# Kernel tuning notes

Hardware: AMD Instinct MI355X
Metric: run time of the kernel (lower is better)

The kernel has to match this reference:

```python
import jax, jax.numpy as jnp
import numpy as np

PSEUDO_CONF_THRES = 0.2


def setup_inputs() -> dict:
    key = jax.random.key(0)
    k1, k2, k3, k4 = jax.random.split(key, 4)
    B, S, M = 4096, 10000, 1000  # batch, num_sub_classes, num_main_classes
    x = jax.random.normal(k1, (B, S), dtype=jnp.float32)
    x_main = jax.random.normal(k2, (B, M), dtype=jnp.float32)
    target = jax.random.randint(k3, (B,), 0, S, dtype=jnp.int64)
    sub2main = jax.random.randint(k4, (S,), 0, M, dtype=jnp.int64)
    return {"x": x, "x_main": x_main, "target": target, "sub2main": sub2main}


def _corrected_target(x, x_main, target, sub2main, thres):
    # Vectorized form of _main2sub_corrected_label (original uses detached scores).
    B, S = x.shape
    score_sub = jax.nn.softmax(x, axis=1)            # [B, S]
    score_main = jax.nn.softmax(x_main, axis=1)      # [B, M]
    pseudo = jnp.argmax(score_sub, axis=1)           # [B]
    rows = jnp.arange(B)
    prob_target = score_main[rows, sub2main[target]]   # [B]
    prob_pseudo = score_main[rows, sub2main[pseudo]]   # [B]
    correct = (target != pseudo) & (prob_pseudo >= thres)
    lam_sum = prob_target + prob_pseudo
    lam_t = jnp.where(correct, prob_target / lam_sum, 1.0)
    lam_c = jnp.where(correct, prob_pseudo / lam_sum, 0.0)
    one_hot = jnp.zeros((B, S), dtype=x.dtype)
    one_hot = one_hot.at[rows, target].add(lam_t)
    one_hot = one_hot.at[rows, pseudo].add(lam_c)
    return one_hot


def reference(x, x_main, target, sub2main):
    corrected = jax.lax.stop_gradient(
        _corrected_target(x, x_main, target, sub2main, PSEUDO_CONF_THRES)
    )
    logp = jax.nn.log_softmax(x, axis=1)             # [B, S]
    loss = jnp.sum(-logp * corrected, axis=1)        # [B]
    return jnp.mean(loss)  # reduction='mean'
```

## Files before the change

### kernel.cpp

```cpp
#include <hip/hip_runtime.h>
#include <float.h>

#define THREADS 256
#define WAVES (THREADS / 64)
#define CONF_THRES 0.2f


typedef float floatx4 __attribute__((ext_vector_type(4)));

__global__ __launch_bounds__(THREADS) void row_loss_kernel(
    const float* __restrict__ x,
    const float* __restrict__ x_main,
    const int* __restrict__ target,
    const int* __restrict__ sub2main,
    float* __restrict__ row_loss,
    int S, int M)
{
    const int b = blockIdx.x;
    const int tid = threadIdx.x;
    const float* __restrict__ xrow = x + (size_t)b * (size_t)S;
    const float* __restrict__ mrow = x_main + (size_t)b * (size_t)M;
    const floatx4* __restrict__ xv = reinterpret_cast<const floatx4*>(xrow);
    const floatx4* __restrict__ mv = reinterpret_cast<const floatx4*>(mrow);
    const int nv  = S >> 2;
    const int mvn = M >> 2;

    const floatx4 fill4 = { -FLT_MAX, -FLT_MAX, -FLT_MAX, -FLT_MAX };

    #define MLOAD(K) ((tid + (K) * THREADS) < nv                               \
                      ? __builtin_nontemporal_load(&xv[tid + (K) * THREADS])   \
                      : fill4)
    floatx4 a0 = MLOAD(0), a1 = MLOAD(1), a2 = MLOAD(2), a3 = MLOAD(3);
    floatx4 b0 = MLOAD(4), b1 = MLOAD(5), b2 = MLOAD(6), b3 = MLOAD(7);
    floatx4 mvec = (tid < mvn) ? __builtin_nontemporal_load(&mv[tid]) : fill4;

    const int   tgt   = target[b];
    const float x_tgt = xrow[tgt];
    const float m_tgt = mrow[sub2main[tgt]];

    float s0 = 0.f, s1 = 0.f, s2 = 0.f, s3 = 0.f;
    float bv0 = -FLT_MAX, bv1 = -FLT_MAX, bv2 = -FLT_MAX, bv3 = -FLT_MAX;
    int   bi0 = 0, bi1 = 0, bi2 = 0, bi3 = 0;

    #define PROC(VEC, K, SS, BV, BI)                                          \
        do {                                                                  \
            floatx4 _v = (VEC); int _b4 = (tid + (K) * THREADS) << 2;         \
            SS += __expf(_v.x) + __expf(_v.y) + __expf(_v.z) + __expf(_v.w);  \
            if (_v.x > BV) { BV = _v.x; BI = _b4;     }                       \
            if (_v.y > BV) { BV = _v.y; BI = _b4 + 1; }                       \
            if (_v.z > BV) { BV = _v.z; BI = _b4 + 2; }                       \
            if (_v.w > BV) { BV = _v.w; BI = _b4 + 3; }                       \
        } while (0)

    PROC(a0, 0, s0, bv0, bi0);
    PROC(a1, 1, s1, bv1, bi1);
    PROC(a2, 2, s2, bv2, bi2);
    PROC(a3, 3, s3, bv3, bi3);
    floatx4 c0 = MLOAD(8);
    floatx4 c1 = MLOAD(9);
    PROC(b0, 4, s0, bv0, bi0);
    PROC(b1, 5, s1, bv1, bi1);
    PROC(b2, 6, s2, bv2, bi2);
    PROC(b3, 7, s3, bv3, bi3);
    PROC(c0, 8, s0, bv0, bi0);
    PROC(c1, 9, s1, bv1, bi1);

    float s_main = __expf(mvec.x) + __expf(mvec.y) +
                   __expf(mvec.z) + __expf(mvec.w);
    #undef PROC
    #undef MLOAD

    float s_sub = (s0 + s1) + (s2 + s3);
    float bv = bv0; int bi = bi0;
    if (bv1 > bv || (bv1 == bv && bi1 < bi)) { bv = bv1; bi = bi1; }
    if (bv2 > bv || (bv2 == bv && bi2 < bi)) { bv = bv2; bi = bi2; }
    if (bv3 > bv || (bv3 == bv && bi3 < bi)) { bv = bv3; bi = bi3; }

    #pragma unroll
    for (int off = 32; off > 0; off >>= 1) {
        s_sub  += __shfl_down(s_sub, off);
        s_main += __shfl_down(s_main, off);
        float v2 = __shfl_down(bv, off);
        int   i2 = __shfl_down(bi, off);
        if (v2 > bv || (v2 == bv && i2 < bi)) { bv = v2; bi = i2; }
    }

    __shared__ float sh_s[WAVES], sh_m[WAVES], sh_bv[WAVES];
    __shared__ int   sh_bi[WAVES];
    const int wid = tid >> 6;
    if ((tid & 63) == 0) {
        sh_s[wid] = s_sub; sh_m[wid] = s_main;
        sh_bv[wid] = bv;   sh_bi[wid] = bi;
    }
    __syncthreads();

    if (tid == 0) {
        #pragma unroll
        for (int w = 1; w < WAVES; ++w) {
            s_sub  += sh_s[w];
            s_main += sh_m[w];
            if (sh_bv[w] > bv || (sh_bv[w] == bv && sh_bi[w] < bi)) {
                bv = sh_bv[w]; bi = sh_bi[w];
            }
        }
        const int pseudo = bi;

        const float logZ   = __logf(s_sub);
        const float logp_t = x_tgt - logZ;
        const float logp_p = bv - logZ;

        const float inv_sm = 1.0f / s_main;
        const float pt = __expf(m_tgt)                  * inv_sm;
        const float pp = __expf(mrow[sub2main[pseudo]]) * inv_sm;

        const bool correct = (tgt != pseudo) && (pp >= CONF_THRES);
        const float inv_lam = 1.0f / (pt + pp);
        const float lam_t = correct ? pt * inv_lam : 1.0f;
        const float lam_c = correct ? pp * inv_lam : 0.0f;

        row_loss[b] = -(lam_t * logp_t + lam_c * logp_p);
    }
}

__global__ __launch_bounds__(THREADS) void mean_kernel(
    const float* __restrict__ rl, float* __restrict__ out, int B)
{
    float acc = 0.0f;
    const int nv = B >> 2;
    const floatx4* __restrict__ rv = reinterpret_cast<const floatx4*>(rl);
    #pragma unroll
    for (int k = 0; k < 4; ++k) {
        int idx = threadIdx.x + k * THREADS;
        if (idx < nv) {
            floatx4 v = rv[idx];
            acc += (v.x + v.y) + (v.z + v.w);
        }
    }
    for (int idx = (nv << 2) + threadIdx.x; idx < B; idx += THREADS)
        acc += rl[idx];
    #pragma unroll
    for (int off = 32; off > 0; off >>= 1) acc += __shfl_down(acc, off);
    __shared__ float w[WAVES];
    if ((threadIdx.x & 63) == 0) w[threadIdx.x >> 6] = acc;
    __syncthreads();
    if (threadIdx.x == 0) {
        float t = 0.0f;
        #pragma unroll
        for (int i = 0; i < WAVES; ++i) t += w[i];
        out[0] = t / (float)B;
    }
}

extern "C" void kernel_launch(void* const* d_in, const int* in_sizes, int n_in,
                              void* d_out, int out_size, void* d_ws, size_t ws_size,
                              hipStream_t stream) {
    const float* x        = (const float*)d_in[0];
    const float* x_main   = (const float*)d_in[1];
    const int*   target   = (const int*)d_in[2];
    const int*   sub2main = (const int*)d_in[3];
    float* out = (float*)d_out;

    const int B = in_sizes[2];
    const int S = in_sizes[3];
    const int M = in_sizes[1] / B;

    float* row_loss = (float*)d_ws;

    row_loss_kernel<<<B, THREADS, 0, stream>>>(x, x_main, target, sub2main,
                                               row_loss, S, M);
    mean_kernel<<<1, THREADS, 0, stream>>>(row_loss, out, B);
}
```

Before: 34.71 us.

## Process two rows per block to halve block count and amortize reductions

```diff
diff --git a/kernel.cpp b/kernel.cpp
--- a/kernel.cpp
+++ b/kernel.cpp
@@ -8,43 +8,47 @@
 
 typedef float floatx4 __attribute__((ext_vector_type(4)));
 
-__global__ __launch_bounds__(THREADS) void row_loss_kernel(
+__global__ __launch_bounds__(THREADS) void row2_loss_kernel(
     const float* __restrict__ x,
     const float* __restrict__ x_main,
     const int* __restrict__ target,
     const int* __restrict__ sub2main,
     float* __restrict__ row_loss,
-    int S, int M)
+    int S, int M, int B)
 {
-    const int b = blockIdx.x;
+    const int b0  = blockIdx.x * 2;
     const int tid = threadIdx.x;
-    const float* __restrict__ xrow = x + (size_t)b * (size_t)S;
-    const float* __restrict__ mrow = x_main + (size_t)b * (size_t)M;
-    const floatx4* __restrict__ xv = reinterpret_cast<const floatx4*>(xrow);
-    const floatx4* __restrict__ mv = reinterpret_cast<const floatx4*>(mrow);
     const int nv  = S >> 2;
     const int mvn = M >> 2;
+    const bool has_r1 = (b0 + 1) < B;
+
+    const float* __restrict__ xrow0 = x + (size_t)b0 * (size_t)S;
+    const float* __restrict__ xrow1 = has_r1 ? xrow0 + S : xrow0;
+    const float* __restrict__ mrow0 = x_main + (size_t)b0 * (size_t)M;
+    const float* __restrict__ mrow1 = has_r1 ? mrow0 + M : mrow0;
+    const floatx4* __restrict__ xv0 = reinterpret_cast<const floatx4*>(xrow0);
+    const floatx4* __restrict__ xv1 = reinterpret_cast<const floatx4*>(xrow1);
+    const floatx4* __restrict__ mv0 = reinterpret_cast<const floatx4*>(mrow0);
+    const floatx4* __restrict__ mv1 = reinterpret_cast<const floatx4*>(mrow1);
+
+    const int tgt0 = target[b0];
+    const int tgt1 = target[has_r1 ? b0 + 1 : b0];
+    const float x_tgt0 = xrow0[tgt0], x_tgt1 = xrow1[tgt1];
+    const float m_tgt0 = mrow0[sub2main[tgt0]];
+    const float m_tgt1 = mrow1[sub2main[tgt1]];
 
     const floatx4 fill4 = { -FLT_MAX, -FLT_MAX, -FLT_MAX, -FLT_MAX };
 
-    #define MLOAD(K) ((tid + (K) * THREADS) < nv                               \
-                      ? __builtin_nontemporal_load(&xv[tid + (K) * THREADS])   \
-                      : fill4)
-    floatx4 a0 = MLOAD(0), a1 = MLOAD(1), a2 = MLOAD(2), a3 = MLOAD(3);
-    floatx4 b0 = MLOAD(4), b1 = MLOAD(5), b2 = MLOAD(6), b3 = MLOAD(7);
-    floatx4 mvec = (tid < mvn) ? __builtin_nontemporal_load(&mv[tid]) : fill4;
+    floatx4 mvec0 = (tid < mvn) ? __builtin_nontemporal_load(&mv0[tid]) : fill4;
+    floatx4 mvec1 = (tid < mvn) ? __builtin_nontemporal_load(&mv1[tid]) : fill4;
 
-    const int   tgt   = target[b];
-    const float x_tgt = xrow[tgt];
-    const float m_tgt = mrow[sub2main[tgt]];
+    float sA0 = 0.f, sA1 = 0.f, sB0 = 0.f, sB1 = 0.f;
+    float bvA0 = -FLT_MAX, bvA1 = -FLT_MAX, bvB0 = -FLT_MAX, bvB1 = -FLT_MAX;
+    int   biA0 = 0, biA1 = 0, biB0 = 0, biB1 = 0;
 
-    float s0 = 0.f, s1 = 0.f, s2 = 0.f, s3 = 0.f;
-    float bv0 = -FLT_MAX, bv1 = -FLT_MAX, bv2 = -FLT_MAX, bv3 = -FLT_MAX;
-    int   bi0 = 0, bi1 = 0, bi2 = 0, bi3 = 0;
-
-    #define PROC(VEC, K, SS, BV, BI)                                          \
+    #define PROC(VEC, BASE4, SS, BV, BI)                                      \
         do {                                                                  \
-            floatx4 _v = (VEC); int _b4 = (tid + (K) * THREADS) << 2;         \
+            floatx4 _v = (VEC); int _b4 = (BASE4);                            \
             SS += __expf(_v.x) + __expf(_v.y) + __expf(_v.z) + __expf(_v.w);  \
             if (_v.x > BV) { BV = _v.x; BI = _b4;     }                       \
             if (_v.y > BV) { BV = _v.y; BI = _b4 + 1; }                       \
@@ -52,58 +56,76 @@
             if (_v.w > BV) { BV = _v.w; BI = _b4 + 3; }                       \
         } while (0)
 
-    PROC(a0, 0, s0, bv0, bi0);
-    PROC(a1, 1, s1, bv1, bi1);
-    PROC(a2, 2, s2, bv2, bi2);
-    PROC(a3, 3, s3, bv3, bi3);
-    floatx4 c0 = MLOAD(8);
-    floatx4 c1 = MLOAD(9);
-    PROC(b0, 4, s0, bv0, bi0);
-    PROC(b1, 5, s1, bv1, bi1);
-    PROC(b2, 6, s2, bv2, bi2);
-    PROC(b3, 7, s3, bv3, bi3);
-    PROC(c0, 8, s0, bv0, bi0);
-    PROC(c1, 9, s1, bv1, bi1);
+    #pragma unroll
+    for (int k = 0; k < 10; ++k) {
+        const int idx = tid + (k << 8);
+        const bool ok = idx < nv;
+        floatx4 vA = ok ? __builtin_nontemporal_load(&xv0[idx]) : fill4;
+        floatx4 vB = ok ? __builtin_nontemporal_load(&xv1[idx]) : fill4;
+        const int base = idx << 2;
+        if (k & 1) {
+            PROC(vA, base, sA1, bvA1, biA1);
+            PROC(vB, base, sB1, bvB1, biB1);
+        } else {
+            PROC(vA, base, sA0, bvA0, biA0);
+            PROC(vB, base, sB0, bvB0, biB0);
+        }
+    }
+    #undef PROC
 
-    float s_main = __expf(mvec.x) + __expf(mvec.y) +
-                   __expf(mvec.z) + __expf(mvec.w);
-    #undef PROC
-    #undef MLOAD
+    float s_main0 = __expf(mvec0.x) + __expf(mvec0.y) +
+                    __expf(mvec0.z) + __expf(mvec0.w);
+    float s_main1 = __expf(mvec1.x) + __expf(mvec1.y) +
+                    __expf(mvec1.z) + __expf(mvec1.w);
 
-    float s_sub = (s0 + s1) + (s2 + s3);
-    float bv = bv0; int bi = bi0;
-    if (bv1 > bv || (bv1 == bv && bi1 < bi)) { bv = bv1; bi = bi1; }
-    if (bv2 > bv || (bv2 == bv && bi2 < bi)) { bv = bv2; bi = bi2; }
-    if (bv3 > bv || (bv3 == bv && bi3 < bi)) { bv = bv3; bi = bi3; }
+    float s_sub0 = sA0 + sA1, s_sub1 = sB0 + sB1;
+    float bv0 = bvA0; int bi0 = biA0;
+    if (bvA1 > bv0 || (bvA1 == bv0 && biA1 < bi0)) { bv0 = bvA1; bi0 = biA1; }
+    float bv1 = bvB0; int bi1 = biB0;
+    if (bvB1 > bv1 || (bvB1 == bv1 && biB1 < bi1)) { bv1 = bvB1; bi1 = biB1; }
 
     #pragma unroll
     for (int off = 32; off > 0; off >>= 1) {
-        s_sub  += __shfl_down(s_sub, off);
-        s_main += __shfl_down(s_main, off);
-        float v2 = __shfl_down(bv, off);
-        int   i2 = __shfl_down(bi, off);
-        if (v2 > bv || (v2 == bv && i2 < bi)) { bv = v2; bi = i2; }
+        s_sub0  += __shfl_down(s_sub0, off);
+        s_sub1  += __shfl_down(s_sub1, off);
+        s_main0 += __shfl_down(s_main0, off);
+        s_main1 += __shfl_down(s_main1, off);
+        float v0 = __shfl_down(bv0, off); int i0 = __shfl_down(bi0, off);
+        if (v0 > bv0 || (v0 == bv0 && i0 < bi0)) { bv0 = v0; bi0 = i0; }
+        float v1 = __shfl_down(bv1, off); int i1 = __shfl_down(bi1, off);
+        if (v1 > bv1 || (v1 == bv1 && i1 < bi1)) { bv1 = v1; bi1 = i1; }
     }
 
-    __shared__ float sh_s[WAVES], sh_m[WAVES], sh_bv[WAVES];
-    __shared__ int   sh_bi[WAVES];
+    __shared__ float sh_s[2][WAVES], sh_m[2][WAVES], sh_bv[2][WAVES];
+    __shared__ int   sh_bi[2][WAVES];
     const int wid = tid >> 6;
     if ((tid & 63) == 0) {
-        sh_s[wid] = s_sub; sh_m[wid] = s_main;
-        sh_bv[wid] = bv;   sh_bi[wid] = bi;
+        sh_s[0][wid] = s_sub0;  sh_s[1][wid] = s_sub1;
+        sh_m[0][wid] = s_main0; sh_m[1][wid] = s_main1;
+        sh_bv[0][wid] = bv0;    sh_bv[1][wid] = bv1;
+        sh_bi[0][wid] = bi0;    sh_bi[1][wid] = bi1;
     }
     __syncthreads();
 
-    if (tid == 0) {
+    if (tid == 0 || (tid == 64 && has_r1)) {
+        const int  r      = (tid == 0) ? 0 : 1;
+        float s_sub  = sh_s[r][0];
+        float s_main = sh_m[r][0];
+        float bv     = sh_bv[r][0];
+        int   bi     = sh_bi[r][0];
         #pragma unroll
         for (int w = 1; w < WAVES; ++w) {
-            s_sub  += sh_s[w];
-            s_main += sh_m[w];
-            if (sh_bv[w] > bv || (sh_bv[w] == bv && sh_bi[w] < bi)) {
-                bv = sh_bv[w]; bi = sh_bi[w];
+            s_sub  += sh_s[r][w];
+            s_main += sh_m[r][w];
+            if (sh_bv[r][w] > bv || (sh_bv[r][w] == bv && sh_bi[r][w] < bi)) {
+                bv = sh_bv[r][w]; bi = sh_bi[r][w];
             }
         }
-        const int pseudo = bi;
+        const int   tgt    = r ? tgt1 : tgt0;
+        const float x_tgt  = r ? x_tgt1 : x_tgt0;
+        const float m_tgt  = r ? m_tgt1 : m_tgt0;
+        const float* mrow  = r ? mrow1 : mrow0;
+        const int   pseudo = bi;
 
         const float logZ   = __logf(s_sub);
         const float logp_t = x_tgt - logZ;
@@ -118,7 +140,7 @@
         const float lam_t = correct ? pt * inv_lam : 1.0f;
         const float lam_c = correct ? pp * inv_lam : 0.0f;
 
-        row_loss[b] = -(lam_t * logp_t + lam_c * logp_p);
+        row_loss[b0 + r] = -(lam_t * logp_t + lam_c * logp_p);
     }
 }
 
@@ -166,7 +188,9 @@
 
     float* row_loss = (float*)d_ws;
 
-    row_loss_kernel<<<B, THREADS, 0, stream>>>(x, x_main, target, sub2main,
-                                               row_loss, S, M);
+    const int nblocks = (B + 1) / 2;
+    row2_loss_kernel<<<nblocks, THREADS, 0, stream>>>(x, x_main, target,
+                                                      sub2main, row_loss,
+                                                      S, M, B);
     mean_kernel<<<1, THREADS, 0, stream>>>(row_loss, out, B);
 }
```

After: 37.47 us. +7.9%, slower.

## Split each softmax row across two blocks and merge halves in finalize

Applied to the files above, without the earlier changes.

```diff
diff --git a/kernel.cpp b/kernel.cpp
--- a/kernel.cpp
+++ b/kernel.cpp
@@ -3,48 +3,63 @@
 
 #define THREADS 256
 #define WAVES (THREADS / 64)
+#define FIN_THREADS 1024
+#define FIN_WAVES (FIN_THREADS / 64)
 #define CONF_THRES 0.2f
 
 
 typedef float floatx4 __attribute__((ext_vector_type(4)));
 
-__global__ __launch_bounds__(THREADS) void row_loss_kernel(
+__global__ __launch_bounds__(THREADS) void half_row_kernel(
     const float* __restrict__ x,
     const float* __restrict__ x_main,
     const int* __restrict__ target,
     const int* __restrict__ sub2main,
-    float* __restrict__ row_loss,
+    floatx4* __restrict__ partial,
     int S, int M)
 {
-    const int b = blockIdx.x;
+    const int blk = blockIdx.x;
+    const int b   = blk >> 1;
+    const int h   = blk & 1;
     const int tid = threadIdx.x;
+    const int nv      = S >> 2;
+    const int half_nv = nv >> 1;
+    const int mvn     = M >> 2;
+
     const float* __restrict__ xrow = x + (size_t)b * (size_t)S;
     const float* __restrict__ mrow = x_main + (size_t)b * (size_t)M;
-    const floatx4* __restrict__ xv = reinterpret_cast<const floatx4*>(xrow);
+    const floatx4* __restrict__ xv =
+        reinterpret_cast<const floatx4*>(xrow) + (size_t)h * half_nv;
     const floatx4* __restrict__ mv = reinterpret_cast<const floatx4*>(mrow);
-    const int nv  = S >> 2;
-    const int mvn = M >> 2;
 
     const floatx4 fill4 = { -FLT_MAX, -FLT_MAX, -FLT_MAX, -FLT_MAX };
 
-    #define MLOAD(K) ((tid + (K) * THREADS) < nv                               \
-                      ? __builtin_nontemporal_load(&xv[tid + (K) * THREADS])   \
+    int tgt = 0; float x_tgt = 0.f, m_tgt = 0.f, s_main = 0.f;
+    if (h == 0) {
+        tgt   = target[b];
+        x_tgt = xrow[tgt];
+        m_tgt = mrow[sub2main[tgt]];
+        floatx4 mvec = (tid < mvn) ? __builtin_nontemporal_load(&mv[tid])
+                                   : fill4;
+        s_main = __expf(mvec.x) + __expf(mvec.y) +
+                 __expf(mvec.z) + __expf(mvec.w);
+    }
+
+    #define MLOAD(K) ((tid + (K) * THREADS) < half_nv                         \
+                      ? __builtin_nontemporal_load(&xv[tid + (K) * THREADS])  \
                       : fill4)
-    floatx4 a0 = MLOAD(0), a1 = MLOAD(1), a2 = MLOAD(2), a3 = MLOAD(3);
-    floatx4 b0 = MLOAD(4), b1 = MLOAD(5), b2 = MLOAD(6), b3 = MLOAD(7);
-    floatx4 mvec = (tid < mvn) ? __builtin_nontemporal_load(&mv[tid]) : fill4;
-
-    const int   tgt   = target[b];
-    const float x_tgt = xrow[tgt];
-    const float m_tgt = mrow[sub2main[tgt]];
+    floatx4 v0 = MLOAD(0), v1 = MLOAD(1), v2 = MLOAD(2), v3 = MLOAD(3);
+    floatx4 v4 = MLOAD(4);
+    #undef MLOAD
 
     float s0 = 0.f, s1 = 0.f, s2 = 0.f, s3 = 0.f;
     float bv0 = -FLT_MAX, bv1 = -FLT_MAX, bv2 = -FLT_MAX, bv3 = -FLT_MAX;
-    int   bi0 = 0, bi1 = 0, bi2 = 0, bi3 = 0;
+    int   bi0 = 0x7fffffff, bi1 = 0x7fffffff, bi2 = 0x7fffffff, bi3 = 0x7fffffff;
 
     #define PROC(VEC, K, SS, BV, BI)                                          \
         do {                                                                  \
-            floatx4 _v = (VEC); int _b4 = (tid + (K) * THREADS) << 2;         \
+            floatx4 _v = (VEC);                                               \
+            int _b4 = (h * half_nv + tid + (K) * THREADS) << 2;               \
             SS += __expf(_v.x) + __expf(_v.y) + __expf(_v.z) + __expf(_v.w);  \
             if (_v.x > BV) { BV = _v.x; BI = _b4;     }                       \
             if (_v.y > BV) { BV = _v.y; BI = _b4 + 1; }                       \
@@ -52,23 +67,12 @@
             if (_v.w > BV) { BV = _v.w; BI = _b4 + 3; }                       \
         } while (0)
 
-    PROC(a0, 0, s0, bv0, bi0);
-    PROC(a1, 1, s1, bv1, bi1);
-    PROC(a2, 2, s2, bv2, bi2);
-    PROC(a3, 3, s3, bv3, bi3);
-    floatx4 c0 = MLOAD(8);
-    floatx4 c1 = MLOAD(9);
-    PROC(b0, 4, s0, bv0, bi0);
-    PROC(b1, 5, s1, bv1, bi1);
-    PROC(b2, 6, s2, bv2, bi2);
-    PROC(b3, 7, s3, bv3, bi3);
-    PROC(c0, 8, s0, bv0, bi0);
-    PROC(c1, 9, s1, bv1, bi1);
-
-    float s_main = __expf(mvec.x) + __expf(mvec.y) +
-                   __expf(mvec.z) + __expf(mvec.w);
+    PROC(v0, 0, s0, bv0, bi0);
+    PROC(v1, 1, s1, bv1, bi1);
+    PROC(v2, 2, s2, bv2, bi2);
+    PROC(v3, 3, s3, bv3, bi3);
+    PROC(v4, 4, s0, bv0, bi0);
     #undef PROC
-    #undef MLOAD
 
     float s_sub = (s0 + s1) + (s2 + s3);
     float bv = bv0; int bi = bi0;
@@ -80,9 +84,9 @@
     for (int off = 32; off > 0; off >>= 1) {
         s_sub  += __shfl_down(s_sub, off);
         s_main += __shfl_down(s_main, off);
-        float v2 = __shfl_down(bv, off);
-        int   i2 = __shfl_down(bi, off);
-        if (v2 > bv || (v2 == bv && i2 < bi)) { bv = v2; bi = i2; }
+        float v2_ = __shfl_down(bv, off);
+        int   i2_ = __shfl_down(bi, off);
+        if (v2_ > bv || (v2_ == bv && i2_ < bi)) { bv = v2_; bi = i2_; }
     }
 
     __shared__ float sh_s[WAVES], sh_m[WAVES], sh_bv[WAVES];
@@ -103,50 +107,59 @@
                 bv = sh_bv[w]; bi = sh_bi[w];
             }
         }
-        const int pseudo = bi;
+        const float mp = mrow[sub2main[bi]];
 
+        floatx4 lo = { s_sub, bv, __int_as_float(bi), mp };
+        floatx4 hi = { s_main, x_tgt, m_tgt, __int_as_float(tgt) };
+        partial[(size_t)blk * 2]     = lo;
+        partial[(size_t)blk * 2 + 1] = hi;
+    }
+}
+
+__global__ __launch_bounds__(FIN_THREADS) void finalize_kernel(
+    const floatx4* __restrict__ partial, float* __restrict__ out, int B)
+{
+    const int tid = threadIdx.x;
+    float acc = 0.0f;
+
+    for (int r = tid; r < B; r += FIN_THREADS) {
+        floatx4 lo0 = partial[(size_t)4 * r];
+        floatx4 hi0 = partial[(size_t)4 * r + 1];
+        floatx4 lo1 = partial[(size_t)4 * r + 2];
+
+        const float s_sub  = lo0.x + lo1.x;
+        const float s_main = hi0.x;
+
+        float bv; int bi; float mp;
+        if (lo1.y > lo0.y) { bv = lo1.y; bi = __float_as_int(lo1.z); mp = lo1.w; }
+        else               { bv = lo0.y; bi = __float_as_int(lo0.z); mp = lo0.w; }
+
+        const int   tgt    = __float_as_int(hi0.w);
         const float logZ   = __logf(s_sub);
-        const float logp_t = x_tgt - logZ;
+        const float logp_t = hi0.y - logZ;
         const float logp_p = bv - logZ;
 
         const float inv_sm = 1.0f / s_main;
-        const float pt = __expf(m_tgt)                  * inv_sm;
-        const float pp = __expf(mrow[sub2main[pseudo]]) * inv_sm;
+        const float pt = __expf(hi0.z) * inv_sm;
+        const float pp = __expf(mp)    * inv_sm;
 
-        const bool correct = (tgt != pseudo) && (pp >= CONF_THRES);
+        const bool correct = (tgt != bi) && (pp >= CONF_THRES);
         const float inv_lam = 1.0f / (pt + pp);
         const float lam_t = correct ? pt * inv_lam : 1.0f;
         const float lam_c = correct ? pp * inv_lam : 0.0f;
 
-        row_loss[b] = -(lam_t * logp_t + lam_c * logp_p);
+        acc += -(lam_t * logp_t + lam_c * logp_p);
     }
-}
 
-__global__ __launch_bounds__(THREADS) void mean_kernel(
-    const float* __restrict__ rl, float* __restrict__ out, int B)
-{
-    float acc = 0.0f;
-    const int nv = B >> 2;
-    const floatx4* __restrict__ rv = reinterpret_cast<const floatx4*>(rl);
-    #pragma unroll
-    for (int k = 0; k < 4; ++k) {
-        int idx = threadIdx.x + k * THREADS;
-        if (idx < nv) {
-            floatx4 v = rv[idx];
-            acc += (v.x + v.y) + (v.z + v.w);
-        }
-    }
-    for (int idx = (nv << 2) + threadIdx.x; idx < B; idx += THREADS)
-        acc += rl[idx];
     #pragma unroll
     for (int off = 32; off > 0; off >>= 1) acc += __shfl_down(acc, off);
-    __shared__ float w[WAVES];
-    if ((threadIdx.x & 63) == 0) w[threadIdx.x >> 6] = acc;
+    __shared__ float w[FIN_WAVES];
+    if ((tid & 63) == 0) w[tid >> 6] = acc;
     __syncthreads();
-    if (threadIdx.x == 0) {
+    if (tid == 0) {
         float t = 0.0f;
         #pragma unroll
-        for (int i = 0; i < WAVES; ++i) t += w[i];
+        for (int i = 0; i < FIN_WAVES; ++i) t += w[i];
         out[0] = t / (float)B;
     }
 }
@@ -164,9 +177,9 @@
     const int S = in_sizes[3];
     const int M = in_sizes[1] / B;
 
-    float* row_loss = (float*)d_ws;
+    floatx4* partial = (floatx4*)d_ws;
 
-    row_loss_kernel<<<B, THREADS, 0, stream>>>(x, x_main, target, sub2main,
-                                               row_loss, S, M);
-    mean_kernel<<<1, THREADS, 0, stream>>>(row_loss, out, B);
+    half_row_kernel<<<B * 2, THREADS, 0, stream>>>(x, x_main, target,
+                                                   sub2main, partial, S, M);
+    finalize_kernel<<<1, FIN_THREADS, 0, stream>>>(partial, out, B);
 }
```

New measurement: 37.05 us. 6.7% more time.
